# Kernel tuning notes

Measured on AMD Instinct MI355X. Metric: run time of the kernel, lower is better.

## Reference

```python
import jax, jax.numpy as jnp
import numpy as np

N = 2048          # num nodes == in_channels (f1 = graphs[0].shape[0])
F_IN = 2048       # node feature dim
G1 = 10           # ChebConv out channels
E = 65536         # num edges (avg degree 32)
NUM_CLASSES = 10  # fc1 output


def setup_inputs() -> dict:
    key = jax.random.key(0)
    ks = jax.random.split(key, 6)
    x = jax.random.normal(ks[0], (N, F_IN), dtype=jnp.float32)
    edge_index = jax.random.randint(ks[1], (2, E), 0, N)
    # ChebConv weights: one [F_IN, G1] matrix per Chebyshev order (K=2), glorot-ish init
    s = float(1.0 / np.sqrt(F_IN))
    W0 = jax.random.uniform(ks[2], (F_IN, G1), jnp.float32, -s, s)
    W1 = jax.random.uniform(ks[3], (F_IN, G1), jnp.float32, -s, s)
    b = jnp.zeros((G1,), jnp.float32)
    sf = float(1.0 / np.sqrt(G1))
    Wf = jax.random.uniform(ks[4], (G1, NUM_CLASSES), jnp.float32, -sf, sf)
    bf = jax.random.uniform(ks[5], (NUM_CLASSES,), jnp.float32, -sf, sf)
    return {"x": x, "edge_index": edge_index, "W0": W0, "W1": W1, "b": b, "Wf": Wf, "bf": bf}


def _cheb_edge_weights(edge_index):
    # PyG ChebConv default: sym-normalized Laplacian scaled with lambda_max=2.0.
    # L_hat = 2*L/lambda_max - I = -D^{-1/2} A D^{-1/2}  (zero diagonal).
    row, col = edge_index[0], edge_index[1]
    deg = jax.ops.segment_sum(jnp.ones((E,), jnp.float32), row, num_segments=N)
    dis = jnp.where(deg > 0, jax.lax.rsqrt(jnp.maximum(deg, 1.0)), 0.0)
    return -dis[row] * dis[col]


def reference(x, edge_index, W0, W1, b, Wf, bf):
    row, col = edge_index[0], edge_index[1]
    w = _cheb_edge_weights(edge_index)
    # Tx_0 = x ; Tx_1 = L_hat @ x via gather (source=row) + scatter-add (target=col)
    Tx1 = jax.ops.segment_sum(w[:, None] * x[row], col, num_segments=N)  # [N, F_IN]
    h = x @ W0 + Tx1 @ W1 + b                                            # ChebConv, K=2
    h = jax.nn.relu(h)
    logits = h @ Wf + bf                                                 # fc1
    return jax.nn.log_softmax(logits, axis=1)
```

## Files before the change

### kernel.cpp

```cpp
#include <hip/hip_runtime.h>

#define N_NODES 2048
#define F_IN    2048
#define G1      10
#define NCLS    10
#define NEDGE   65536
#define JCHUNKS 64
#define JPER    32
#define HSLICES 128
#define ZSLICES 64

__device__ float g_p[JCHUNKS * 20 * N_NODES];
__device__ int   g_degp[HSLICES * N_NODES];
__device__ float g_dis[N_NODES];
__device__ float g_y[N_NODES * 20];
__device__ float g_zp[2 * ZSLICES * N_NODES * 5];
__device__ float g_z[N_NODES * G1];

__global__ __launch_bounds__(256) void k_gemm(const float* __restrict__ x,
                                              const float* __restrict__ W0,
                                              const float* __restrict__ W1,
                                              const int* __restrict__ ei) {
    __shared__ float sx[256 * 33];
    int jc      = blockIdx.x;
    int rowbase = blockIdx.y * 256;
    int j0      = jc * JPER;

    #pragma unroll
    for (int rep = 0; rep < 8; ++rep) {
        int idx = rep * 256 + threadIdx.x;
        int r = idx >> 3, c4 = idx & 7;
        float4 v = *(const float4*)(x + (size_t)(rowbase + r) * F_IN + j0 + c4 * 4);
        float* d = sx + r * 33 + c4 * 4;
        d[0] = v.x; d[1] = v.y; d[2] = v.z; d[3] = v.w;
    }
    __syncthreads();

    float acc[20];
    #pragma unroll
    for (int k = 0; k < 20; ++k) acc[k] = 0.f;

    const float* xr = sx + threadIdx.x * 33;
    #pragma unroll
    for (int j = 0; j < JPER; ++j) {
        float xu = xr[j];
        const float* w0r = W0 + (size_t)(j0 + j) * G1;
        const float* w1r = W1 + (size_t)(j0 + j) * G1;
        #pragma unroll
        for (int k = 0; k < G1; ++k) {
            acc[k]      += xu * w0r[k];
            acc[10 + k] += xu * w1r[k];
        }
    }
    int row = rowbase + threadIdx.x;
    #pragma unroll
    for (int k = 0; k < 20; ++k)
        g_p[((size_t)jc * 20 + k) * N_NODES + row] = acc[k];

    if (blockIdx.y < 4) {
        int hs = blockIdx.y * JCHUNKS + jc;
        hs = blockIdx.y * 64 + jc;
        hs = (blockIdx.y << 5) * 2 + jc;
        hs = blockIdx.y * 32 + (jc & 31);
        if (jc < 32) {
            int slice = blockIdx.y * 32 + jc;
            __syncthreads();
            int* h = (int*)sx;
            #pragma unroll
            for (int t = threadIdx.x; t < N_NODES; t += 256) h[t] = 0;
            __syncthreads();
            int base = slice * (NEDGE / HSLICES);
            #pragma unroll
            for (int u = 0; u < 2; ++u)
                atomicAdd(&h[ei[base + u * 256 + threadIdx.x]], 1);
            __syncthreads();
            #pragma unroll
            for (int t = threadIdx.x; t < N_NODES; t += 256)
                g_degp[slice * N_NODES + t] = h[t];
        }
    }
}

__global__ __launch_bounds__(256) void k_reduce() {
    int t   = blockIdx.x * 256 + threadIdx.x;
    int k   = t >> 11;
    int row = t & (N_NODES - 1);
    float s = 0.f;
    #pragma unroll 16
    for (int jc = 0; jc < JCHUNKS; ++jc)
        s += g_p[((size_t)jc * 20 + k) * N_NODES + row];
    g_y[row * 20 + k] = s;
    if (t < N_NODES) {
        int d = 0;
        #pragma unroll 16
        for (int sl = 0; sl < HSLICES; ++sl) d += g_degp[sl * N_NODES + t];
        g_dis[t] = (d > 0) ? rsqrtf((float)d) : 0.f;
    }
}

__global__ __launch_bounds__(256) void k_scatter(const int* __restrict__ ei) {
    __shared__ float zl[N_NODES * 5];
    int khalf  = blockIdx.x >> 6;
    int bslice = blockIdx.x & (ZSLICES - 1);
    float4* zl4 = (float4*)zl;
    #pragma unroll
    for (int t = threadIdx.x; t < N_NODES * 5 / 4; t += 256)
        zl4[t] = make_float4(0.f, 0.f, 0.f, 0.f);
    __syncthreads();
    int base = bslice * (NEDGE / ZSLICES);
    #pragma unroll
    for (int u = 0; u < NEDGE / ZSLICES / 256; ++u) {
        int e = base + u * 256 + threadIdx.x;
        int r = ei[e], c = ei[NEDGE + e];
        float w = -g_dis[r] * g_dis[c];
        const float* y1 = g_y + r * 20 + 10 + khalf * 5;
        float* zz = zl + c * 5;
        #pragma unroll
        for (int kk = 0; kk < 5; ++kk) atomicAdd(&zz[kk], w * y1[kk]);
    }
    __syncthreads();
    float4* dst = (float4*)(g_zp + ((size_t)khalf * ZSLICES + bslice) * (N_NODES * 5));
    #pragma unroll
    for (int t = threadIdx.x; t < N_NODES * 5 / 4; t += 256) dst[t] = zl4[t];
}

__global__ __launch_bounds__(256) void k_zred() {
    int t = blockIdx.x * 256 + threadIdx.x;
    int khalf = t / (N_NODES * 5);
    int rem   = t % (N_NODES * 5);
    float s = 0.f;
    #pragma unroll 16
    for (int sl = 0; sl < ZSLICES; ++sl)
        s += g_zp[((size_t)khalf * ZSLICES + sl) * (N_NODES * 5) + rem];
    int i = rem / 5, kk = rem - i * 5;
    g_z[i * 10 + khalf * 5 + kk] = s;
}

__global__ __launch_bounds__(256) void k_final(const float* __restrict__ b,
                                               const float* __restrict__ Wf,
                                               const float* __restrict__ bfv,
                                               float* __restrict__ out) {
    int i = blockIdx.x * 256 + threadIdx.x;
    float h[G1];
    #pragma unroll
    for (int k = 0; k < G1; ++k)
        h[k] = fmaxf(g_y[i * 20 + k] + g_z[i * 10 + k] + b[k], 0.f);
    float lo[NCLS];
    #pragma unroll
    for (int c = 0; c < NCLS; ++c) lo[c] = bfv[c];
    #pragma unroll
    for (int k = 0; k < G1; ++k) {
        float hk = h[k];
        #pragma unroll
        for (int c = 0; c < NCLS; ++c) lo[c] += hk * Wf[k * NCLS + c];
    }
    float m = lo[0];
    #pragma unroll
    for (int c = 1; c < NCLS; ++c) m = fmaxf(m, lo[c]);
    float s = 0.f;
    #pragma unroll
    for (int c = 0; c < NCLS; ++c) s += expf(lo[c] - m);
    float ls = logf(s);
    #pragma unroll
    for (int c = 0; c < NCLS; ++c) out[i * NCLS + c] = lo[c] - m - ls;
}

extern "C" void kernel_launch(void* const* d_in, const int* in_sizes, int n_in,
                              void* d_out, int out_size, void* d_ws, size_t ws_size,
                              hipStream_t stream) {
    const float* x   = (const float*)d_in[0];
    const int*   ei  = (const int*)d_in[1];
    const float* W0  = (const float*)d_in[2];
    const float* W1  = (const float*)d_in[3];
    const float* b   = (const float*)d_in[4];
    const float* Wf  = (const float*)d_in[5];
    const float* bfv = (const float*)d_in[6];
    float* out = (float*)d_out;

    k_gemm<<<dim3(JCHUNKS, N_NODES / 256), 256, 0, stream>>>(x, W0, W1, ei);
    k_reduce<<<(N_NODES * 20) / 256, 256, 0, stream>>>();
    k_scatter<<<2 * ZSLICES, 256, 0, stream>>>(ei);
    k_zred<<<(N_NODES * G1) / 256, 256, 0, stream>>>();
    k_final<<<N_NODES / 256, 256, 0, stream>>>(b, Wf, bfv, out);
}
```

Before: 110.8 us.

## Fuse z-reduction into final softmax kernel and halve GEMM partial chunks

The separate z-slice reduction kernel is merged into the final ChebConv/fc/log-softmax kernel: each block reduces the scatter partials for 32 nodes into shared memory and then computes the outputs. This removes one launch and the g_z round trip through global memory. Separately, the GEMM now handles 64 input columns per block in two 32-column halves, so there are 32 chunks and k_reduce reads half as many partials. The cost is a smaller GEMM grid (256 blocks), and the fused final kernel has only 64 blocks with just 32 active threads in the softmax phase.

```diff
diff --git a/kernel.cpp b/kernel.cpp
--- a/kernel.cpp
+++ b/kernel.cpp
@@ -5,8 +5,8 @@
 #define G1      10
 #define NCLS    10
 #define NEDGE   65536
-#define JCHUNKS 64
-#define JPER    32
+#define JCHUNKS 32
+#define JPER    64
 #define HSLICES 128
 #define ZSLICES 64
 
@@ -15,7 +15,6 @@
 __device__ float g_dis[N_NODES];
 __device__ float g_y[N_NODES * 20];
 __device__ float g_zp[2 * ZSLICES * N_NODES * 5];
-__device__ float g_z[N_NODES * G1];
 
 __global__ __launch_bounds__(256) void k_gemm(const float* __restrict__ x,
                                               const float* __restrict__ W0,
@@ -24,32 +23,35 @@
     __shared__ float sx[256 * 33];
     int jc      = blockIdx.x;
     int rowbase = blockIdx.y * 256;
-    int j0      = jc * JPER;
-
-    #pragma unroll
-    for (int rep = 0; rep < 8; ++rep) {
-        int idx = rep * 256 + threadIdx.x;
-        int r = idx >> 3, c4 = idx & 7;
-        float4 v = *(const float4*)(x + (size_t)(rowbase + r) * F_IN + j0 + c4 * 4);
-        float* d = sx + r * 33 + c4 * 4;
-        d[0] = v.x; d[1] = v.y; d[2] = v.z; d[3] = v.w;
-    }
-    __syncthreads();
 
     float acc[20];
     #pragma unroll
     for (int k = 0; k < 20; ++k) acc[k] = 0.f;
 
-    const float* xr = sx + threadIdx.x * 33;
     #pragma unroll
-    for (int j = 0; j < JPER; ++j) {
-        float xu = xr[j];
-        const float* w0r = W0 + (size_t)(j0 + j) * G1;
-        const float* w1r = W1 + (size_t)(j0 + j) * G1;
+    for (int half = 0; half < 2; ++half) {
+        int j0 = jc * JPER + half * 32;
+        if (half) __syncthreads();
         #pragma unroll
-        for (int k = 0; k < G1; ++k) {
-            acc[k]      += xu * w0r[k];
-            acc[10 + k] += xu * w1r[k];
+        for (int rep = 0; rep < 8; ++rep) {
+            int idx = rep * 256 + threadIdx.x;
+            int r = idx >> 3, c4 = idx & 7;
+            float4 v = *(const float4*)(x + (size_t)(rowbase + r) * F_IN + j0 + c4 * 4);
+            float* d = sx + r * 33 + c4 * 4;
+            d[0] = v.x; d[1] = v.y; d[2] = v.z; d[3] = v.w;
+        }
+        __syncthreads();
+        const float* xr = sx + threadIdx.x * 33;
+        #pragma unroll
+        for (int j = 0; j < 32; ++j) {
+            float xu = xr[j];
+            const float* w0r = W0 + (size_t)(j0 + j) * G1;
+            const float* w1r = W1 + (size_t)(j0 + j) * G1;
+            #pragma unroll
+            for (int k = 0; k < G1; ++k) {
+                acc[k]      += xu * w0r[k];
+                acc[10 + k] += xu * w1r[k];
+            }
         }
     }
     int row = rowbase + threadIdx.x;
@@ -58,26 +60,18 @@
         g_p[((size_t)jc * 20 + k) * N_NODES + row] = acc[k];
 
     if (blockIdx.y < 4) {
-        int hs = blockIdx.y * JCHUNKS + jc;
-        hs = blockIdx.y * 64 + jc;
-        hs = (blockIdx.y << 5) * 2 + jc;
-        hs = blockIdx.y * 32 + (jc & 31);
-        if (jc < 32) {
-            int slice = blockIdx.y * 32 + jc;
-            __syncthreads();
-            int* h = (int*)sx;
-            #pragma unroll
-            for (int t = threadIdx.x; t < N_NODES; t += 256) h[t] = 0;
-            __syncthreads();
-            int base = slice * (NEDGE / HSLICES);
-            #pragma unroll
-            for (int u = 0; u < 2; ++u)
-                atomicAdd(&h[ei[base + u * 256 + threadIdx.x]], 1);
-            __syncthreads();
-            #pragma unroll
-            for (int t = threadIdx.x; t < N_NODES; t += 256)
-                g_degp[slice * N_NODES + t] = h[t];
-        }
+        int slice = blockIdx.y * 32 + jc;
+        __syncthreads();
+        int* h = (int*)sx;
+        for (int t = threadIdx.x; t < N_NODES; t += 256) h[t] = 0;
+        __syncthreads();
+        int base = slice * (NEDGE / HSLICES);
+        #pragma unroll
+        for (int u = 0; u < 2; ++u)
+            atomicAdd(&h[ei[base + u * 256 + threadIdx.x]], 1);
+        __syncthreads();
+        for (int t = threadIdx.x; t < N_NODES; t += 256)
+            g_degp[slice * N_NODES + t] = h[t];
     }
 }
 
@@ -124,45 +118,48 @@
     for (int t = threadIdx.x; t < N_NODES * 5 / 4; t += 256) dst[t] = zl4[t];
 }
 
-__global__ __launch_bounds__(256) void k_zred() {
-    int t = blockIdx.x * 256 + threadIdx.x;
-    int khalf = t / (N_NODES * 5);
-    int rem   = t % (N_NODES * 5);
-    float s = 0.f;
-    #pragma unroll 16
-    for (int sl = 0; sl < ZSLICES; ++sl)
-        s += g_zp[((size_t)khalf * ZSLICES + sl) * (N_NODES * 5) + rem];
-    int i = rem / 5, kk = rem - i * 5;
-    g_z[i * 10 + khalf * 5 + kk] = s;
-}
-
-__global__ __launch_bounds__(256) void k_final(const float* __restrict__ b,
-                                               const float* __restrict__ Wf,
-                                               const float* __restrict__ bfv,
-                                               float* __restrict__ out) {
-    int i = blockIdx.x * 256 + threadIdx.x;
-    float h[G1];
-    #pragma unroll
-    for (int k = 0; k < G1; ++k)
-        h[k] = fmaxf(g_y[i * 20 + k] + g_z[i * 10 + k] + b[k], 0.f);
-    float lo[NCLS];
-    #pragma unroll
-    for (int c = 0; c < NCLS; ++c) lo[c] = bfv[c];
-    #pragma unroll
-    for (int k = 0; k < G1; ++k) {
-        float hk = h[k];
+__global__ __launch_bounds__(256) void k_zf(const float* __restrict__ b,
+                                            const float* __restrict__ Wf,
+                                            const float* __restrict__ bfv,
+                                            float* __restrict__ out) {
+    __shared__ float zb[320];
+    int nb = blockIdx.x * 32;
+    for (int v = threadIdx.x; v < 320; v += 256) {
+        int khalf = v / 160;
+        int rem   = v - khalf * 160;
+        int il    = rem / 5, kk = rem - il * 5;
+        float s = 0.f;
+        #pragma unroll 16
+        for (int sl = 0; sl < ZSLICES; ++sl)
+            s += g_zp[((size_t)khalf * ZSLICES + sl) * (N_NODES * 5) + (nb + il) * 5 + kk];
+        zb[il * 10 + khalf * 5 + kk] = s;
+    }
+    __syncthreads();
+    if (threadIdx.x < 32) {
+        int i = nb + threadIdx.x;
+        float h[G1];
         #pragma unroll
-        for (int c = 0; c < NCLS; ++c) lo[c] += hk * Wf[k * NCLS + c];
+        for (int k = 0; k < G1; ++k)
+            h[k] = fmaxf(g_y[i * 20 + k] + zb[threadIdx.x * 10 + k] + b[k], 0.f);
+        float lo[NCLS];
+        #pragma unroll
+        for (int c = 0; c < NCLS; ++c) lo[c] = bfv[c];
+        #pragma unroll
+        for (int k = 0; k < G1; ++k) {
+            float hk = h[k];
+            #pragma unroll
+            for (int c = 0; c < NCLS; ++c) lo[c] += hk * Wf[k * NCLS + c];
+        }
+        float m = lo[0];
+        #pragma unroll
+        for (int c = 1; c < NCLS; ++c) m = fmaxf(m, lo[c]);
+        float s = 0.f;
+        #pragma unroll
+        for (int c = 0; c < NCLS; ++c) s += expf(lo[c] - m);
+        float ls = logf(s);
+        #pragma unroll
+        for (int c = 0; c < NCLS; ++c) out[i * NCLS + c] = lo[c] - m - ls;
     }
-    float m = lo[0];
-    #pragma unroll
-    for (int c = 1; c < NCLS; ++c) m = fmaxf(m, lo[c]);
-    float s = 0.f;
-    #pragma unroll
-    for (int c = 0; c < NCLS; ++c) s += expf(lo[c] - m);
-    float ls = logf(s);
-    #pragma unroll
-    for (int c = 0; c < NCLS; ++c) out[i * NCLS + c] = lo[c] - m - ls;
 }
 
 extern "C" void kernel_launch(void* const* d_in, const int* in_sizes, int n_in,
@@ -180,6 +177,5 @@
     k_gemm<<<dim3(JCHUNKS, N_NODES / 256), 256, 0, stream>>>(x, W0, W1, ei);
     k_reduce<<<(N_NODES * 20) / 256, 256, 0, stream>>>();
     k_scatter<<<2 * ZSLICES, 256, 0, stream>>>(ei);
-    k_zred<<<(N_NODES * G1) / 256, 256, 0, stream>>>();
-    k_final<<<N_NODES / 256, 256, 0, stream>>>(b, Wf, bfv, out);
+    k_zf<<<N_NODES / 32, 256, 0, stream>>>(b, Wf, bfv, out);
 }
```

New measurement: 115.1 us. 3.9% more time.
